# Optimization experiments

Hardware: AMD Instinct MI355X
Metric: run time of the kernel (lower is better)

The kernel has to match this reference:

```python
import jax, jax.numpy as jnp
import numpy as np
import math

N_HEADS = 16
ROPE_BASE = 10000.0


def _rope_interleaved(t, cos, sin):
    # t: [B,H,T,dk]; cos/sin: [T, dk//2] broadcast over B,H
    te, to = t[..., 0::2], t[..., 1::2]
    re = te * cos - to * sin
    ro = te * sin + to * cos
    # interleave back: [..., dk//2, 2] -> [..., dk]
    return jnp.stack([re, ro], axis=-1).reshape(t.shape)


def setup_inputs() -> dict:
    key = jax.random.key(0)
    ks = jax.random.split(key, 5)
    B, T, C = 2, 2048, 1024
    s = 1.0 / math.sqrt(C)
    return {
        "x": jax.random.normal(ks[0], (B, T, C), dtype=jnp.float32),
        "W_qkv": jax.random.normal(ks[1], (C, 3 * C), dtype=jnp.float32) * s,
        "b_qkv": jax.random.normal(ks[2], (3 * C,), dtype=jnp.float32) * 0.02,
        "W_proj": jax.random.normal(ks[3], (C, C), dtype=jnp.float32) * s,
        "b_proj": jax.random.normal(ks[4], (C,), dtype=jnp.float32) * 0.02,
    }


def reference(x, W_qkv, b_qkv, W_proj, b_proj):
    B, T, C = x.shape
    H = N_HEADS
    dk = C // H

    qkv = x @ W_qkv + b_qkv                      # [B,T,3C]
    q, k, v = jnp.split(qkv, 3, axis=-1)
    q = q.reshape(B, T, H, dk).transpose(0, 2, 1, 3)  # [B,H,T,dk]
    k = k.reshape(B, T, H, dk).transpose(0, 2, 1, 3)
    v = v.reshape(B, T, H, dk).transpose(0, 2, 1, 3)

    # RoPE angles: pos * base^(-2i/dk)
    freqs = ROPE_BASE ** (-2.0 * jnp.arange(dk // 2, dtype=jnp.float32) / dk)
    angles = jnp.arange(T, dtype=jnp.float32)[:, None] * freqs[None, :]  # [T,dk//2]
    cos, sin = jnp.cos(angles), jnp.sin(angles)

    q = _rope_interleaved(q, cos, sin)
    k = _rope_interleaved(k, cos, sin)

    attn = jnp.einsum("bhqd,bhkd->bhqk", q, k) / math.sqrt(dk)  # [B,H,T,T]
    causal = jnp.triu(jnp.full((T, T), -jnp.inf, dtype=attn.dtype), k=1)
    attn = jax.nn.softmax(attn + causal, axis=-1)

    scores = jnp.einsum("bhqk,bhkd->bhqd", attn, v)  # [B,H,T,dk]
    scores = scores.transpose(0, 2, 1, 3).reshape(B, T, C)
    return scores @ W_proj + b_proj
```

## Files before the change

### kernel.cpp

```cpp
#include <hip/hip_runtime.h>
#include <hip/hip_bf16.h>

typedef __bf16 bf16x8 __attribute__((ext_vector_type(8)));
typedef float f32x4 __attribute__((ext_vector_type(4)));
typedef float f32x16 __attribute__((ext_vector_type(16)));
typedef unsigned short u16;
typedef u16 u16x8 __attribute__((ext_vector_type(8)));

__device__ __forceinline__ u16 f2bf(float f) {
  union { float f; unsigned u; } v; v.f = f;
  unsigned r = v.u + 0x7fffu + ((v.u >> 16) & 1u);
  return (u16)(r >> 16);
}
__device__ __forceinline__ float bf2f(u16 u) {
  union { unsigned u; float f; } v; v.u = (unsigned)u << 16; return v.f;
}
__device__ __forceinline__ unsigned cvtpk(float a, float b) {
  unsigned r;
  asm("v_cvt_pk_bf16_f32 %0, %1, %2" : "=v"(r) : "v"(a), "v"(b));
  return r;
}
__device__ __forceinline__ float exp2_(float x) {
  float r;
  asm("v_exp_f32 %0, %1" : "=v"(r) : "v"(x));
  return r;
}
__device__ __forceinline__ float sin2pi_(float x) {
  float r;
  asm("v_sin_f32 %0, %1" : "=v"(r) : "v"(x));
  return r;
}
__device__ __forceinline__ float cos2pi_(float x) {
  float r;
  asm("v_cos_f32 %0, %1" : "=v"(r) : "v"(x));
  return r;
}
__device__ __forceinline__ void gload16(const void* g, void* l) {
  __builtin_amdgcn_global_load_lds(
      (__attribute__((address_space(1))) void*)(void*)g,
      (__attribute__((address_space(3))) void*)l, 16, 0, 0);
}

union U8 { bf16x8 v; unsigned u[4]; };

__global__ __launch_bounds__(256) void cast_x_k(const float* __restrict__ x,
                                                u16* __restrict__ xb, int n8) {
  int id = blockIdx.x * 256 + threadIdx.x;
  if (id >= n8) return;
  const float4* p = (const float4*)(x + (size_t)id * 8);
  float4 a = p[0], b = p[1];
  u16x8 o;
  o[0] = f2bf(a.x); o[1] = f2bf(a.y); o[2] = f2bf(a.z); o[3] = f2bf(a.w);
  o[4] = f2bf(b.x); o[5] = f2bf(b.y); o[6] = f2bf(b.z); o[7] = f2bf(b.w);
  *(u16x8*)(xb + (size_t)id * 8) = o;
}

__global__ __launch_bounds__(256) void tcast_k(const float* __restrict__ W,
                                               u16* __restrict__ Wt, int R, int Cc) {
  __shared__ float tile[32][33];
  int bx = blockIdx.x * 32, by = blockIdx.y * 32;
  int tx = threadIdx.x & 31, ty = threadIdx.x >> 5;
#pragma unroll
  for (int j = 0; j < 4; j++)
    tile[ty + j * 8][tx] = W[(size_t)(by + ty + j * 8) * Cc + bx + tx];
  __syncthreads();
#pragma unroll
  for (int j = 0; j < 4; j++)
    Wt[(size_t)(bx + ty + j * 8) * R + by + tx] = f2bf(tile[tx][ty + j * 8]);
}

template <bool BF16OUT>
__global__ __launch_bounds__(256) void gemm_bt_k(const u16* __restrict__ A,
                                                 const u16* __restrict__ Bt,
                                                 const float* __restrict__ bias,
                                                 void* __restrict__ Cv,
                                                 int M, int N, int K) {
  __shared__ u16 As[128 * 64];
  __shared__ u16 Bs[128 * 64];
  int tid = threadIdx.x;
  int m0 = blockIdx.y * 128, n0 = blockIdx.x * 128;
  int wave = tid >> 6, lane = tid & 63;
  int wm = (wave & 1) * 64, wn = (wave >> 1) * 64;
  int lrow = lane & 15, lk = (lane >> 4) * 8;
  int rr = lane >> 3, cb = (lane & 7) * 16;

  f32x4 acc[4][4] = {};

  for (int k0 = 0; k0 < K; k0 += 64) {
#pragma unroll
    for (int i = 0; i < 4; i++) {
      int row = wave * 32 + i * 8 + rr;
      int cc = (cb ^ ((row & 7) << 4)) >> 1;
      gload16(A + (size_t)(m0 + row) * K + k0 + cc, &As[(wave * 32 + i * 8) * 64]);
      gload16(Bt + (size_t)(n0 + row) * K + k0 + cc, &Bs[(wave * 32 + i * 8) * 64]);
    }
    __syncthreads();
#pragma unroll
    for (int kk = 0; kk < 2; kk++) {
      bf16x8 af[4], bfr[4];
#pragma unroll
      for (int i = 0; i < 4; i++) {
        int arow = wm + i * 16 + lrow;
        int ab = (arow * 128 + (kk * 32 + lk) * 2) ^ ((arow & 7) << 4);
        af[i] = *(const bf16x8*)((const char*)As + ab);
        int brow = wn + i * 16 + lrow;
        int bb = (brow * 128 + (kk * 32 + lk) * 2) ^ ((brow & 7) << 4);
        bfr[i] = *(const bf16x8*)((const char*)Bs + bb);
      }
#pragma unroll
      for (int i = 0; i < 4; i++)
#pragma unroll
        for (int j = 0; j < 4; j++)
          acc[i][j] = __builtin_amdgcn_mfma_f32_16x16x32_bf16(af[i], bfr[j], acc[i][j], 0, 0, 0);
    }
    __syncthreads();
  }
  int rg = lane >> 4;
#pragma unroll
  for (int i = 0; i < 4; i++) {
#pragma unroll
    for (int j = 0; j < 4; j++) {
      int col = n0 + wn + j * 16 + lrow;
      float bz = bias ? bias[col] : 0.f;
#pragma unroll
      for (int r = 0; r < 4; r++) {
        int row = m0 + wm + i * 16 + rg * 4 + r;
        float val = acc[i][j][r] + bz;
        if constexpr (BF16OUT)
          ((u16*)Cv)[(size_t)row * N + col] = f2bf(val);
        else
          ((float*)Cv)[(size_t)row * N + col] = val;
      }
    }
  }
}

__global__ __launch_bounds__(256) void rope_pack_k(const u16* __restrict__ qkv,
                                                   u16* __restrict__ qf,
                                                   u16* __restrict__ kf,
                                                   u16* __restrict__ vf) {
  __shared__ u16 tl[64][72];
  int bh = blockIdx.x, tb = blockIdx.y;
  int b = bh >> 4, h = bh & 15;
  int tid = threadIdx.x;
  int tloc = tid >> 2;
  int a = tid & 3;
  int tg = tb * 64 + tloc;
  const u16* rowp = qkv + ((size_t)(b * 2048 + tg)) * 3072 + h * 64 + 16 * a;
  u16x8 q0 = *(const u16x8*)(rowp);
  u16x8 q1 = *(const u16x8*)(rowp + 8);
  u16x8 k0 = *(const u16x8*)(rowp + 1024);
  u16x8 k1 = *(const u16x8*)(rowp + 1032);
  const float QS = 0.18033688011112042f;
  const float C1 = -0.41524101186092029f;
  const float C2 = 0.15915494309189535f;
  u16x8 qo0, qo1, ko0, ko1;
#pragma unroll
  for (int j = 0; j < 8; j++) {
    int i = 8 * a + j;
    float fr = (float)tg * (exp2f((float)i * C1) * C2);
    fr = fr - floorf(fr);
    float sv = sin2pi_(fr), cv = cos2pi_(fr);
    float qx, qy, kx, ky;
    if (j < 4) {
      qx = bf2f(q0[2 * j]); qy = bf2f(q0[2 * j + 1]);
      kx = bf2f(k0[2 * j]); ky = bf2f(k0[2 * j + 1]);
    } else {
      qx = bf2f(q1[2 * j - 8]); qy = bf2f(q1[2 * j - 7]);
      kx = bf2f(k1[2 * j - 8]); ky = bf2f(k1[2 * j - 7]);
    }
    u16 qre = f2bf((qx * cv - qy * sv) * QS), qro = f2bf((qx * sv + qy * cv) * QS);
    u16 kre = f2bf(kx * cv - ky * sv),        kro = f2bf(kx * sv + ky * cv);
    if (j < 4) { qo0[2 * j] = qre; qo0[2 * j + 1] = qro; ko0[2 * j] = kre; ko0[2 * j + 1] = kro; }
    else       { qo1[2 * j - 8] = qre; qo1[2 * j - 7] = qro; ko1[2 * j - 8] = kre; ko1[2 * j - 7] = kro; }
  }
  size_t qbase = ((size_t)bh * 64 + (tg >> 5)) * 2048 + a * 512 + (tg & 31) * 8;
  *(u16x8*)(qf + qbase) = qo0;
  *(u16x8*)(qf + qbase + 256) = qo1;
  size_t kbase = (((size_t)bh * 32 + (tg >> 6)) * 2 + ((tg >> 5) & 1)) * 2048 + a * 512 + (tg & 31) * 8;
  *(u16x8*)(kf + kbase) = ko0;
  *(u16x8*)(kf + kbase + 256) = ko1;
#pragma unroll
  for (int rep = 0; rep < 2; rep++) {
    int tr = rep * 32 + (tid >> 3);
    int dc = (tid & 7) * 8;
    u16x8 v = *(const u16x8*)(qkv + ((size_t)(b * 2048 + tb * 64 + tr)) * 3072 + 2048 + h * 64 + dc);
    *(u16x8*)&tl[tr][dc] = v;
  }
  __syncthreads();
  u16* dst = vf + ((size_t)bh * 32 + tb) * 4096;
#pragma unroll
  for (int rep = 0; rep < 2; rep++) {
    int c = rep * 256 + tid;
    int dh = c >> 8, s = (c >> 6) & 3, l = c & 63;
    int hi = l >> 5, ql = l & 31;
    u16x8 o;
#pragma unroll
    for (int j = 0; j < 8; j++) o[j] = tl[s * 16 + hi * 8 + j][dh * 32 + ql];
    *(u16x8*)(dst + (size_t)c * 8) = o;
  }
}

__global__ __launch_bounds__(64, 4) void attn_k(const u16* __restrict__ Qf,
                                                const u16* __restrict__ Kf,
                                                const u16* __restrict__ Vf,
                                                u16* __restrict__ sc,
                                                u16* __restrict__ pO,
                                                float* __restrict__ pL) {
  const int T = 2048;
  int blk = blockIdx.x;
  int bh = (blk & 7) * 4 + ((blk >> 3) & 3);
  int c = blk >> 5;
  int qt, slot, nslots;
  if (c < 64)       { qt = 63 - (c >> 2);              slot = c & 3;        nslots = 4; }
  else if (c < 112) { int cc = c - 64; int d3 = cc / 3; qt = 47 - d3;       slot = cc - 3 * d3; nslots = 3; }
  else if (c < 144) { int cc = c - 112; qt = 31 - (cc >> 1); slot = cc & 1; nslots = 2; }
  else              { qt = 159 - c;                    slot = 0;            nslots = 1; }
  int nIter = qt + 1;
  int it0 = (nIter * slot) / nslots;
  int itEnd = (nIter * (slot + 1)) / nslots;
  int lane = threadIdx.x & 63;
  int ql = lane & 31, hi = lane >> 5;
  int ln8 = lane * 8;
  int qg = qt * 32 + ql;
  const u16* QfP = Qf + (size_t)bh * 64 * 2048;
  const u16* KfP = Kf + (size_t)bh * 64 * 2048;
  const u16* VfP = Vf + (size_t)bh * 32 * 4096;
  int b = bh >> 4, h = bh & 15;

  U8 onesf;
#pragma unroll
  for (int j = 0; j < 4; j++) onesf.u[j] = 0x3F803F80u;

  bf16x8 qfr[4];
#pragma unroll
  for (int ds = 0; ds < 4; ds++)
    qfr[ds] = *(const bf16x8*)(QfP + (size_t)qt * 2048 + ds * 512 + ln8);

  f32x16 o0 = {}, o1 = {}, ls = {};

  for (int t = it0; t < itEnd; ++t) {
    const u16* kb = KfP + (size_t)t * 2048 + ln8;
    bf16x8 k0 = *(const bf16x8*)(kb);
    bf16x8 k1 = *(const bf16x8*)(kb + 512);
    bf16x8 k2 = *(const bf16x8*)(kb + 1024);
    bf16x8 k3 = *(const bf16x8*)(kb + 1536);
    f32x16 S = {};
    S = __builtin_amdgcn_mfma_f32_32x32x16_bf16(k0, qfr[0], S, 0, 0, 0);
    S = __builtin_amdgcn_mfma_f32_32x32x16_bf16(k1, qfr[1], S, 0, 0, 0);
    S = __builtin_amdgcn_mfma_f32_32x32x16_bf16(k2, qfr[2], S, 0, 0, 0);
    S = __builtin_amdgcn_mfma_f32_32x32x16_bf16(k3, qfr[3], S, 0, 0, 0);
    const u16* vb = VfP + (size_t)(t >> 1) * 4096 + (t & 1) * 1024 + ln8;
    bf16x8 v00 = *(const bf16x8*)(vb);
    bf16x8 v01 = *(const bf16x8*)(vb + 512);
    bf16x8 v10 = *(const bf16x8*)(vb + 2048);
    bf16x8 v11 = *(const bf16x8*)(vb + 2560);
    if (t == nIter - 1) {
      int kv0 = t * 32;
#pragma unroll
      for (int r = 0; r < 16; r++) {
        int k = kv0 + ((r & 3) + 8 * (r >> 2) + 4 * hi);
        if (k > qg) S[r] = -3e38f;
      }
    }
#pragma unroll
    for (int r = 0; r < 16; r++) S[r] = exp2_(S[r]);
    unsigned w0 = cvtpk(S[0], S[1]),   w1 = cvtpk(S[2], S[3]);
    unsigned w2 = cvtpk(S[4], S[5]),   w3 = cvtpk(S[6], S[7]);
    unsigned w4 = cvtpk(S[8], S[9]),   w5 = cvtpk(S[10], S[11]);
    unsigned w6 = cvtpk(S[12], S[13]), w7 = cvtpk(S[14], S[15]);
    asm("v_permlane32_swap_b32 %0, %1" : "+v"(w0), "+v"(w2));
    asm("v_permlane32_swap_b32 %0, %1" : "+v"(w1), "+v"(w3));
    asm("v_permlane32_swap_b32 %0, %1" : "+v"(w4), "+v"(w6));
    asm("v_permlane32_swap_b32 %0, %1" : "+v"(w5), "+v"(w7));
    U8 pf0, pf1;
    pf0.u[0] = w0; pf0.u[1] = w1; pf0.u[2] = w2; pf0.u[3] = w3;
    pf1.u[0] = w4; pf1.u[1] = w5; pf1.u[2] = w6; pf1.u[3] = w7;
    o0 = __builtin_amdgcn_mfma_f32_32x32x16_bf16(v00, pf0.v, o0, 0, 0, 0);
    o0 = __builtin_amdgcn_mfma_f32_32x32x16_bf16(v01, pf1.v, o0, 0, 0, 0);
    o1 = __builtin_amdgcn_mfma_f32_32x32x16_bf16(v10, pf0.v, o1, 0, 0, 0);
    o1 = __builtin_amdgcn_mfma_f32_32x32x16_bf16(v11, pf1.v, o1, 0, 0, 0);
    ls = __builtin_amdgcn_mfma_f32_32x32x16_bf16(onesf.v, pf0.v, ls, 0, 0, 0);
    ls = __builtin_amdgcn_mfma_f32_32x32x16_bf16(onesf.v, pf1.v, ls, 0, 0, 0);
  }

  if (nslots == 1) {
    float inv = 1.f / ls[0];
    u16* orow = sc + ((size_t)(b * T + qg)) * 1024 + h * 64;
#pragma unroll
    for (int j = 0; j < 4; j++) {
      ushort4 o;
      o.x = f2bf(o0[4 * j + 0] * inv); o.y = f2bf(o0[4 * j + 1] * inv);
      o.z = f2bf(o0[4 * j + 2] * inv); o.w = f2bf(o0[4 * j + 3] * inv);
      *(ushort4*)(orow + 8 * j + 4 * hi) = o;
      ushort4 q2;
      q2.x = f2bf(o1[4 * j + 0] * inv); q2.y = f2bf(o1[4 * j + 1] * inv);
      q2.z = f2bf(o1[4 * j + 2] * inv); q2.w = f2bf(o1[4 * j + 3] * inv);
      *(ushort4*)(orow + 32 + 8 * j + 4 * hi) = q2;
    }
  } else {
    u16* orow = pO + (size_t)slot * 4194304 + ((size_t)(b * T + qg)) * 1024 + h * 64;
#pragma unroll
    for (int j = 0; j < 4; j++) {
      ushort4 o;
      o.x = f2bf(o0[4 * j + 0]); o.y = f2bf(o0[4 * j + 1]);
      o.z = f2bf(o0[4 * j + 2]); o.w = f2bf(o0[4 * j + 3]);
      *(ushort4*)(orow + 8 * j + 4 * hi) = o;
      ushort4 q2;
      q2.x = f2bf(o1[4 * j + 0]); q2.y = f2bf(o1[4 * j + 1]);
      q2.z = f2bf(o1[4 * j + 2]); q2.w = f2bf(o1[4 * j + 3]);
      *(ushort4*)(orow + 32 + 8 * j + 4 * hi) = q2;
    }
    if (hi == 0) pL[slot * 65536 + bh * 2048 + qg] = ls[0];
  }
}

__global__ __launch_bounds__(256) void mrg_k(const u16* __restrict__ pO,
                                             const float* __restrict__ pL,
                                             u16* __restrict__ sc) {
  int id = blockIdx.x * 256 + threadIdx.x;
  int col8 = id & 127;
  int rp = id >> 7;
  int b = (rp >= 1536) ? 1 : 0;
  int t = 512 + rp - b * 1536;
  int h = col8 >> 3;
  int qt = t >> 5;
  int ns = (qt >= 48) ? 4 : (qt >= 32) ? 3 : 2;
  int bh = b * 16 + h;
  size_t idx8 = ((size_t)(b * 2048 + t) * 128 + col8);
  float acc[8] = {};
  float lsum = 0.f;
  for (int s = 0; s < ns; s++) {
    lsum += pL[s * 65536 + bh * 2048 + t];
    u16x8 v = *(const u16x8*)(pO + (size_t)s * 4194304 + idx8 * 8);
#pragma unroll
    for (int j = 0; j < 8; j++) acc[j] += bf2f(v[j]);
  }
  float inv = 1.f / lsum;
  u16x8 o;
#pragma unroll
  for (int j = 0; j < 8; j++) o[j] = f2bf(acc[j] * inv);
  *(u16x8*)(sc + idx8 * 8) = o;
}

extern "C" void kernel_launch(void* const* d_in, const int* in_sizes, int n_in,
                              void* d_out, int out_size, void* d_ws, size_t ws_size,
                              hipStream_t stream) {
  const float* x      = (const float*)d_in[0];
  const float* W_qkv  = (const float*)d_in[1];
  const float* b_qkv  = (const float*)d_in[2];
  const float* W_proj = (const float*)d_in[3];
  const float* b_proj = (const float*)d_in[4];
  float* out = (float*)d_out;

  const int B = 2, T = 2048, C = 1024;
  const int M = B * T;

  char* ws = (char*)d_ws;
  u16* wprojt = (u16*)(ws);
  u16* xb     = (u16*)(ws + (2ull << 20));
  u16* wqkvt  = (u16*)(ws + (10ull << 20));
  u16* qkvb   = (u16*)(ws + (16ull << 20));
  u16* pO     = (u16*)(ws + (2ull << 20));
  float* pL   = (float*)(ws + (34ull << 20));
  u16* qfb    = (u16*)(ws + (40ull << 20));
  u16* kfb    = (u16*)(ws + (48ull << 20));
  u16* vfb    = (u16*)(ws + (56ull << 20));
  u16* sc     = (u16*)(ws + (64ull << 20));

  cast_x_k<<<(M * C / 8 + 255) / 256, 256, 0, stream>>>(x, xb, M * C / 8);
  tcast_k<<<dim3(3 * C / 32, C / 32), 256, 0, stream>>>(W_qkv, wqkvt, C, 3 * C);
  tcast_k<<<dim3(C / 32, C / 32), 256, 0, stream>>>(W_proj, wprojt, C, C);
  gemm_bt_k<true><<<dim3(3 * C / 128, M / 128), 256, 0, stream>>>(xb, wqkvt, b_qkv, qkvb, M, 3 * C, C);
  rope_pack_k<<<dim3(B * 16, T / 64), 256, 0, stream>>>(qkvb, qfb, kfb, vfb);
  attn_k<<<5120, 64, 0, stream>>>(qfb, kfb, vfb, sc, pO, pL);
  mrg_k<<<1536, 256, 0, stream>>>(pO, pL, sc);
  gemm_bt_k<false><<<dim3(C / 128, M / 128), 256, 0, stream>>>(sc, wprojt, b_proj, out, M, C, C);
}
```

Measured before the change: 121.2 us.

## Add triple-buffered async-load GEMM with XCD-aware block remap for QKV projection

New measurement: 123.5 us. No clear change (+1.9%).

```diff
diff --git a/kernel.cpp b/kernel.cpp
--- a/kernel.cpp
+++ b/kernel.cpp
@@ -121,6 +121,85 @@
 #pragma unroll
     for (int j = 0; j < 4; j++) {
       int col = n0 + wn + j * 16 + lrow;
+      float bz = bias ? bias[col] : 0.f;
+#pragma unroll
+      for (int r = 0; r < 4; r++) {
+        int row = m0 + wm + i * 16 + rg * 4 + r;
+        float val = acc[i][j][r] + bz;
+        if constexpr (BF16OUT)
+          ((u16*)Cv)[(size_t)row * N + col] = f2bf(val);
+        else
+          ((float*)Cv)[(size_t)row * N + col] = val;
+      }
+    }
+  }
+}
+
+template <bool BF16OUT>
+__global__ __launch_bounds__(256, 2) void gemm3_k(const u16* __restrict__ A,
+                                                  const u16* __restrict__ Bt,
+                                                  const float* __restrict__ bias,
+                                                  void* __restrict__ Cv,
+                                                  int M, int N, int K) {
+  __shared__ u16 As[3][128 * 32];
+  __shared__ u16 Bs[3][128 * 32];
+  int tid = threadIdx.x;
+  int wid = tid >> 6, lane = tid & 63;
+  int nbx = N >> 7;
+  int nwg = (M >> 7) * nbx;
+  int wg = (blockIdx.x & 7) * (nwg >> 3) + (blockIdx.x >> 3);
+  int m0 = (wg / nbx) * 128, n0 = (wg % nbx) * 128;
+  int wm = (wid & 1) * 64, wn = (wid >> 1) * 64;
+  int srow = lane >> 2;
+  int cswz = ((lane & 3) ^ (srow & 3)) * 8;
+  int r0 = wid * 16;
+  int frow = lane & 15;
+  int fch = ((lane >> 4) ^ (frow & 3)) * 8;
+
+#define G3_STAGE(KT, BUF)                                                         \
+  do {                                                                            \
+    gload16(A + (size_t)(m0 + r0 + srow) * K + (KT) * 32 + cswz,                  \
+            &As[BUF][r0 * 32]);                                                   \
+    gload16(A + (size_t)(m0 + 64 + r0 + srow) * K + (KT) * 32 + cswz,             \
+            &As[BUF][(64 + r0) * 32]);                                            \
+    gload16(Bt + (size_t)(n0 + r0 + srow) * K + (KT) * 32 + cswz,                 \
+            &Bs[BUF][r0 * 32]);                                                   \
+    gload16(Bt + (size_t)(n0 + 64 + r0 + srow) * K + (KT) * 32 + cswz,            \
+            &Bs[BUF][(64 + r0) * 32]);                                            \
+  } while (0)
+
+  f32x4 acc[4][4] = {};
+  const int KT = K >> 5;
+  G3_STAGE(0, 0);
+  G3_STAGE(1, 1);
+#pragma unroll 1
+  for (int kt = 0; kt < KT; ++kt) {
+    __builtin_amdgcn_s_barrier();
+    if (kt + 1 < KT) asm volatile("s_waitcnt vmcnt(4)" ::: "memory");
+    else             asm volatile("s_waitcnt vmcnt(0)" ::: "memory");
+    __builtin_amdgcn_sched_barrier(0);
+    if (kt + 2 < KT) G3_STAGE(kt + 2, (kt + 2) % 3);
+    const u16* la = As[kt % 3];
+    const u16* lb = Bs[kt % 3];
+    bf16x8 af[4], bfr[4];
+#pragma unroll
+    for (int i = 0; i < 4; i++) {
+      af[i]  = *(const bf16x8*)(la + (wm + i * 16 + frow) * 32 + fch);
+      bfr[i] = *(const bf16x8*)(lb + (wn + i * 16 + frow) * 32 + fch);
+    }
+#pragma unroll
+    for (int i = 0; i < 4; i++)
+#pragma unroll
+      for (int j = 0; j < 4; j++)
+        acc[i][j] = __builtin_amdgcn_mfma_f32_16x16x32_bf16(af[i], bfr[j], acc[i][j], 0, 0, 0);
+  }
+#undef G3_STAGE
+  int rg = lane >> 4;
+#pragma unroll
+  for (int i = 0; i < 4; i++) {
+#pragma unroll
+    for (int j = 0; j < 4; j++) {
+      int col = n0 + wn + j * 16 + frow;
       float bz = bias ? bias[col] : 0.f;
 #pragma unroll
       for (int r = 0; r < 4; r++) {
@@ -371,7 +450,7 @@
   cast_x_k<<<(M * C / 8 + 255) / 256, 256, 0, stream>>>(x, xb, M * C / 8);
   tcast_k<<<dim3(3 * C / 32, C / 32), 256, 0, stream>>>(W_qkv, wqkvt, C, 3 * C);
   tcast_k<<<dim3(C / 32, C / 32), 256, 0, stream>>>(W_proj, wprojt, C, C);
-  gemm_bt_k<true><<<dim3(3 * C / 128, M / 128), 256, 0, stream>>>(xb, wqkvt, b_qkv, qkvb, M, 3 * C, C);
+  gemm3_k<true><<<(M / 128) * (3 * C / 128), 256, 0, stream>>>(xb, wqkvt, b_qkv, qkvb, M, 3 * C, C);
   rope_pack_k<<<dim3(B * 16, T / 64), 256, 0, stream>>>(qkvb, qfb, kfb, vfb);
   attn_k<<<5120, 64, 0, stream>>>(qfb, kfb, vfb, sc, pO, pL);
   mrg_k<<<1536, 256, 0, stream>>>(pO, pL, sc);
```
